# Kernel tuning notes

Hardware: AMD Instinct MI355X
Metric: run time of the kernel (lower is better)

The kernel has to match this reference:

```python
import jax, jax.numpy as jnp
import numpy as np

ANCHOR_NUM = 8
CLASS_NUM = 2
IN_DIM = 1024

def setup_inputs() -> dict:
    key = jax.random.key(0)
    k1, k2, k3, k4 = jax.random.split(key, 4)
    batch_input = jax.random.normal(k1, (64, 512, IN_DIM), dtype=jnp.float32)
    # labels in {-1, 0, 1}: -1 = padding, 0 = negative anchor, 1 = positive anchor
    anchor_labels = jax.random.randint(k2, (64, 512, ANCHOR_NUM), 0, 3, dtype=jnp.int64 if jax.config.read('jax_enable_x64') else jnp.int32) - 1
    lim = 1.0 / np.sqrt(IN_DIM)
    W = jax.random.uniform(k3, (IN_DIM, ANCHOR_NUM * CLASS_NUM), dtype=jnp.float32, minval=-lim, maxval=lim)
    b = jax.random.uniform(k4, (ANCHOR_NUM * CLASS_NUM,), dtype=jnp.float32, minval=-lim, maxval=lim)
    return {"batch_input": batch_input, "W": W, "b": b, "anchor_labels": anchor_labels}

def reference(batch_input, W, b, anchor_labels):
    B, S, _ = batch_input.shape
    # logits: (B, S, anchor_num, class_num)
    logits = (jnp.einsum('bsd,dk->bsk', batch_input, W) + b).reshape(B, S, ANCHOR_NUM, CLASS_NUM)
    predict_label = jnp.argmax(logits, axis=3)  # (B, S, A)
    valid = (anchor_labels != -1)
    labels = jnp.maximum(anchor_labels, 0)  # safe class index for padded entries
    logp = jax.nn.log_softmax(logits, axis=-1)
    nll = -jnp.take_along_axis(logp, labels[..., None].astype(jnp.int32), axis=-1)[..., 0]
    # CrossEntropyLoss (mean) over all non-padding anchors == eval-path gather + CE
    vf = valid.astype(logits.dtype)
    loss = jnp.sum(nll * vf) / jnp.maximum(jnp.sum(vf), 1.0)
    # candidate mask stands in for candidate_idx (positive predictions, non-padding)
    candidate_mask = (predict_label == 1) & valid
    return loss, predict_label, candidate_mask
```

## Files before the change

### kernel.cpp

```cpp
#include <hip/hip_runtime.h>
#include <math.h>


#define ROWS 64
#define NWAVE 4
#define DWAVE 256
#define CHUNK 32
#define XPAD 33

__global__ __launch_bounds__(256, 3)
void rpn_main(const float* __restrict__ x, const float* __restrict__ W,
              const float* __restrict__ b, const int* __restrict__ lab,
              float* __restrict__ out, float* __restrict__ ws)
{
    __shared__ float xs[NWAVE][ROWS * XPAD];
    __shared__ float red[ROWS][NWAVE * 16 + 4];

    const int tid  = threadIdx.x;
    const int wave = tid >> 6;
    const int lane = tid & 63;
    const int row0 = blockIdx.x * ROWS;

    const int uwave = __builtin_amdgcn_readfirstlane(wave);
    const float* __restrict__ Wp = W + (size_t)uwave * DWAVE * 16;

    const float* __restrict__ gbase = x + (size_t)row0 * 1024 + (size_t)wave * DWAVE;

    float acc[16];
#pragma unroll
    for (int c = 0; c < 16; ++c) acc[c] = 0.f;

    for (int ch = 0; ch < DWAVE / CHUNK; ++ch) {
        const float* gsrc = gbase + ch * CHUNK;
#pragma unroll
        for (int j = 0; j < 8; ++j) {
            int fl = j * 64 + lane;
            int r  = fl >> 3;
            int c4 = fl & 7;
            float4 v = *(const float4*)(gsrc + (size_t)r * 1024 + c4 * 4);
            float* dst = &xs[wave][r * XPAD + c4 * 4];
            dst[0] = v.x; dst[1] = v.y; dst[2] = v.z; dst[3] = v.w;
        }
        __syncthreads();

        const float* __restrict__ Wc = Wp + ch * CHUNK * 16;
        const float* xrow = &xs[wave][lane * XPAD];
#pragma unroll 4
        for (int dd = 0; dd < CHUNK; ++dd) {
            float xv = xrow[dd];
#pragma unroll
            for (int c = 0; c < 16; ++c)
                acc[c] = fmaf(xv, Wc[dd * 16 + c], acc[c]);
        }
        __syncthreads();
    }

#pragma unroll
    for (int c = 0; c < 16; c += 4) {
        float4 v = make_float4(acc[c], acc[c + 1], acc[c + 2], acc[c + 3]);
        *(float4*)&red[lane][wave * 16 + c] = v;
    }
    __syncthreads();

    if (tid < 64) {
        const int row = row0 + tid;
        float L[16];
#pragma unroll
        for (int c = 0; c < 16; ++c)
            L[c] = red[tid][c] + red[tid][16 + c] + red[tid][32 + c] + red[tid][48 + c]
                 + b[c];

        const int*  labp  = lab + (size_t)row * 8;
        float*      predp = out + 1 + (size_t)row * 8;
        float*      maskp = out + 1 + 262144 + (size_t)row * 8;

        float lsum = 0.f, lcnt = 0.f;
#pragma unroll
        for (int a = 0; a < 8; ++a) {
            float l0 = L[2 * a], l1 = L[2 * a + 1];
            int   lb = labp[a];
            int   pred  = (l1 > l0) ? 1 : 0;
            int   valid = (lb != -1);
            float m   = fmaxf(l0, l1);
            float lse = m + logf(expf(l0 - m) + expf(l1 - m));
            float nll = lse - ((lb == 1) ? l1 : l0);
            if (valid) { lsum += nll; lcnt += 1.f; }
            predp[a] = (float)pred;
            maskp[a] = (pred && valid) ? 1.f : 0.f;
        }

#pragma unroll
        for (int off = 32; off > 0; off >>= 1) {
            lsum += __shfl_down(lsum, off);
            lcnt += __shfl_down(lcnt, off);
        }
        if (tid == 0) {
            atomicAdd(&ws[0], lsum);
            atomicAdd(&ws[1], lcnt);
        }
    }
}

__global__ void rpn_final(const float* __restrict__ ws, float* __restrict__ out)
{
    out[0] = ws[0] / fmaxf(ws[1], 1.f);
}

extern "C" void kernel_launch(void* const* d_in, const int* in_sizes, int n_in,
                              void* d_out, int out_size, void* d_ws, size_t ws_size,
                              hipStream_t stream)
{
    const float* x   = (const float*)d_in[0];
    const float* W   = (const float*)d_in[1];
    const float* b   = (const float*)d_in[2];
    const int*   lab = (const int*)d_in[3];
    float* out = (float*)d_out;
    float* ws  = (float*)d_ws;

    hipMemsetAsync(ws, 0, 2 * sizeof(float), stream);
    rpn_main<<<dim3(512), dim3(256), 0, stream>>>(x, W, b, lab, out, ws);
    rpn_final<<<dim3(1), dim3(1), 0, stream>>>(ws, out);
}
```

Before: 234.4 us.

## Halve rows per block, split output columns across half-waves, stage W in LDS

Each block now handles 32 rows instead of 64, and the grid doubles to 1024 blocks. Within a wave, the two 32-lane halves each compute 8 of the 16 logit columns for the same row. W chunks are staged into shared memory and read with vectorized float4 loads, and the x tile is stored and read as float4 with a stride of 36. The goal is more blocks and occupancy to pull more memory bandwidth from this memory-bound 128MB read, and fewer scalar LDS and W loads; the cost is W being reloaded into LDS by every block.

```diff
diff --git a/kernel.cpp b/kernel.cpp
--- a/kernel.cpp
+++ b/kernel.cpp
@@ -2,77 +2,95 @@
 #include <math.h>
 
 
-#define ROWS 64
-#define NWAVE 4
-#define DWAVE 256
-#define CHUNK 32
-#define XPAD 33
+#define ROWS   32
+#define NW     4
+#define KSLICE 256
+#define CHUNK  32
+#define XSTR   36
 
-__global__ __launch_bounds__(256, 3)
+__global__ __launch_bounds__(256, 4)
 void rpn_main(const float* __restrict__ x, const float* __restrict__ W,
               const float* __restrict__ b, const int* __restrict__ lab,
               float* __restrict__ out, float* __restrict__ ws)
 {
-    __shared__ float xs[NWAVE][ROWS * XPAD];
-    __shared__ float red[ROWS][NWAVE * 16 + 4];
+    __shared__ float xs[NW * ROWS * XSTR];
+    __shared__ float wch[NW * CHUNK * 16];
+    float* red = xs;
 
     const int tid  = threadIdx.x;
     const int wave = tid >> 6;
     const int lane = tid & 63;
+    const int r    = lane & 31;
+    const int h    = lane >> 5;
     const int row0 = blockIdx.x * ROWS;
 
-    const int uwave = __builtin_amdgcn_readfirstlane(wave);
-    const float* __restrict__ Wp = W + (size_t)uwave * DWAVE * 16;
+    float* xslab = xs + wave * (ROWS * XSTR);
+    const float* gx = x + (size_t)row0 * 1024 + wave * KSLICE;
 
-    const float* __restrict__ gbase = x + (size_t)row0 * 1024 + (size_t)wave * DWAVE;
+    float acc[8];
+#pragma unroll
+    for (int c = 0; c < 8; ++c) acc[c] = 0.f;
 
-    float acc[16];
+    for (int ch = 0; ch < KSLICE / CHUNK; ++ch) {
+        const float* gsrc = gx + ch * CHUNK;
 #pragma unroll
-    for (int c = 0; c < 16; ++c) acc[c] = 0.f;
-
-    for (int ch = 0; ch < DWAVE / CHUNK; ++ch) {
-        const float* gsrc = gbase + ch * CHUNK;
+        for (int j = 0; j < 4; ++j) {
+            int fl = j * 64 + lane;
+            int rr = fl >> 3;
+            int c4 = fl & 7;
+            float4 v = *(const float4*)(gsrc + (size_t)rr * 1024 + c4 * 4);
+            *(float4*)(xslab + rr * XSTR + c4 * 4) = v;
+        }
 #pragma unroll
-        for (int j = 0; j < 8; ++j) {
-            int fl = j * 64 + lane;
-            int r  = fl >> 3;
-            int c4 = fl & 7;
-            float4 v = *(const float4*)(gsrc + (size_t)r * 1024 + c4 * 4);
-            float* dst = &xs[wave][r * XPAD + c4 * 4];
-            dst[0] = v.x; dst[1] = v.y; dst[2] = v.z; dst[3] = v.w;
+        for (int j = 0; j < 2; ++j) {
+            int e = (tid + 256 * j) * 4;
+            float4 wv = *(const float4*)(W + e + (e >> 9) * 3584 + ch * 512);
+            *(float4*)(wch + e) = wv;
         }
         __syncthreads();
 
-        const float* __restrict__ Wc = Wp + ch * CHUNK * 16;
-        const float* xrow = &xs[wave][lane * XPAD];
-#pragma unroll 4
-        for (int dd = 0; dd < CHUNK; ++dd) {
-            float xv = xrow[dd];
+        const float* xrow = xslab + r * XSTR;
+        const float* wp   = wch + wave * (CHUNK * 16) + h * 8;
 #pragma unroll
-            for (int c = 0; c < 16; ++c)
-                acc[c] = fmaf(xv, Wc[dd * 16 + c], acc[c]);
+        for (int t4 = 0; t4 < 8; ++t4) {
+            float4 xq = *(const float4*)(xrow + t4 * 4);
+#pragma unroll
+            for (int i = 0; i < 4; ++i) {
+                int dd = t4 * 4 + i;
+                float xv = (&xq.x)[i];
+                float4 w0 = *(const float4*)(wp + dd * 16);
+                float4 w1 = *(const float4*)(wp + dd * 16 + 4);
+                acc[0] = fmaf(xv, w0.x, acc[0]);
+                acc[1] = fmaf(xv, w0.y, acc[1]);
+                acc[2] = fmaf(xv, w0.z, acc[2]);
+                acc[3] = fmaf(xv, w0.w, acc[3]);
+                acc[4] = fmaf(xv, w1.x, acc[4]);
+                acc[5] = fmaf(xv, w1.y, acc[5]);
+                acc[6] = fmaf(xv, w1.z, acc[6]);
+                acc[7] = fmaf(xv, w1.w, acc[7]);
+            }
         }
         __syncthreads();
     }
 
-#pragma unroll
-    for (int c = 0; c < 16; c += 4) {
-        float4 v = make_float4(acc[c], acc[c + 1], acc[c + 2], acc[c + 3]);
-        *(float4*)&red[lane][wave * 16 + c] = v;
+    {
+        float* rp = red + r * 68 + wave * 16 + h * 8;
+        *(float4*)(rp)     = make_float4(acc[0], acc[1], acc[2], acc[3]);
+        *(float4*)(rp + 4) = make_float4(acc[4], acc[5], acc[6], acc[7]);
     }
     __syncthreads();
 
-    if (tid < 64) {
+    if (tid < ROWS) {
         const int row = row0 + tid;
         float L[16];
 #pragma unroll
         for (int c = 0; c < 16; ++c)
-            L[c] = red[tid][c] + red[tid][16 + c] + red[tid][32 + c] + red[tid][48 + c]
-                 + b[c];
+            L[c] = red[tid * 68 + c] + red[tid * 68 + 16 + c]
+                 + red[tid * 68 + 32 + c] + red[tid * 68 + 48 + c] + b[c];
 
-        const int*  labp  = lab + (size_t)row * 8;
-        float*      predp = out + 1 + (size_t)row * 8;
-        float*      maskp = out + 1 + 262144 + (size_t)row * 8;
+        const int* labp  = lab + (size_t)row * 8;
+        float*     predp = out + 1 + (size_t)row * 8;
+        float*     maskp = out + 1 + 262144 + (size_t)row * 8;
 
         float lsum = 0.f, lcnt = 0.f;
 #pragma unroll
@@ -90,9 +108,9 @@
         }
 
 #pragma unroll
-        for (int off = 32; off > 0; off >>= 1) {
-            lsum += __shfl_down(lsum, off);
-            lcnt += __shfl_down(lcnt, off);
+        for (int off = 16; off > 0; off >>= 1) {
+            lsum += __shfl_down(lsum, off, 32);
+            lcnt += __shfl_down(lcnt, off, 32);
         }
         if (tid == 0) {
             atomicAdd(&ws[0], lsum);
@@ -118,6 +136,6 @@
     float* ws  = (float*)d_ws;
 
     hipMemsetAsync(ws, 0, 2 * sizeof(float), stream);
-    rpn_main<<<dim3(512), dim3(256), 0, stream>>>(x, W, b, lab, out, ws);
+    rpn_main<<<dim3(1024), dim3(256), 0, stream>>>(x, W, b, lab, out, ws);
     rpn_final<<<dim3(1), dim3(1), 0, stream>>>(ws, out);
 }
```

After: 217.5 us. -7.2%, faster.

## Retile GEMV into 32-row blocks with register prefetch and LDS-staged W

Applied to the files above, without the earlier changes.

Restructures the matmul so each block handles 32 rows across the full K dimension in 128-wide chunks. Each thread computes an 8x8 register tile using float4 LDS reads, W is staged in LDS, and the next x chunk is prefetched into registers while the current one is computed. The grid doubles to 1024 blocks, and cross-thread K partials are combined with LDS atomics. The epilogue uses all 256 threads, one per anchor, with a block-level loss reduction before the global atomic. The aim is more memory-level parallelism and fewer LDS reads per FMA on a bandwidth-bound 128MB read, at the cost of many LDS float atomics.

```diff
diff --git a/kernel.cpp b/kernel.cpp
--- a/kernel.cpp
+++ b/kernel.cpp
@@ -2,102 +2,129 @@
 #include <math.h>
 
 
-#define ROWS 64
-#define NWAVE 4
-#define DWAVE 256
-#define CHUNK 32
-#define XPAD 33
+#define ROWS 32
+#define CK   128
+#define NCH  8
 
-__global__ __launch_bounds__(256, 3)
+__global__ __launch_bounds__(256, 4)
 void rpn_main(const float* __restrict__ x, const float* __restrict__ W,
               const float* __restrict__ b, const int* __restrict__ lab,
               float* __restrict__ out, float* __restrict__ ws)
 {
-    __shared__ float xs[NWAVE][ROWS * XPAD];
-    __shared__ float red[ROWS][NWAVE * 16 + 4];
+    __shared__ __align__(16) float xs[ROWS * CK];
+    __shared__ __align__(16) float wlds[CK * 16];
+    __shared__ float red[ROWS * 16];
+    __shared__ float lossred[2];
 
-    const int tid  = threadIdx.x;
-    const int wave = tid >> 6;
-    const int lane = tid & 63;
+    const int tid = threadIdx.x;
+    const int g   = tid >> 3;
+    const int rg  = (tid & 7) >> 1;
+    const int cg  = tid & 1;
     const int row0 = blockIdx.x * ROWS;
 
-    const int uwave = __builtin_amdgcn_readfirstlane(wave);
-    const float* __restrict__ Wp = W + (size_t)uwave * DWAVE * 16;
+    red[tid]       = b[tid & 15];
+    red[tid + 256] = b[tid & 15];
+    if (tid < 2) lossred[tid] = 0.f;
 
-    const float* __restrict__ gbase = x + (size_t)row0 * 1024 + (size_t)wave * DWAVE;
+    const float* gx = x + (size_t)row0 * 1024;
 
-    float acc[16];
+    float acc[8][8];
 #pragma unroll
-    for (int c = 0; c < 16; ++c) acc[c] = 0.f;
+    for (int i = 0; i < 8; ++i)
+#pragma unroll
+        for (int c = 0; c < 8; ++c) acc[i][c] = 0.f;
 
-    for (int ch = 0; ch < DWAVE / CHUNK; ++ch) {
-        const float* gsrc = gbase + ch * CHUNK;
+    float4 xv[4];
 #pragma unroll
-        for (int j = 0; j < 8; ++j) {
-            int fl = j * 64 + lane;
-            int r  = fl >> 3;
-            int c4 = fl & 7;
-            float4 v = *(const float4*)(gsrc + (size_t)r * 1024 + c4 * 4);
-            float* dst = &xs[wave][r * XPAD + c4 * 4];
-            dst[0] = v.x; dst[1] = v.y; dst[2] = v.z; dst[3] = v.w;
+    for (int j = 0; j < 4; ++j) {
+        int fl = j * 256 + tid;
+        xv[j] = *(const float4*)(gx + (size_t)(fl >> 5) * 1024 + (fl & 31) * 4);
+    }
+
+    for (int c = 0; c < NCH; ++c) {
+        __syncthreads();
+#pragma unroll
+        for (int j = 0; j < 4; ++j)
+            *(float4*)(xs + (j * 256 + tid) * 4) = xv[j];
+#pragma unroll
+        for (int j = 0; j < 2; ++j) {
+            int fl = j * 256 + tid;
+            float4 wv = *(const float4*)(W + c * (CK * 16) + fl * 4);
+            *(float4*)(wlds + fl * 4) = wv;
         }
         __syncthreads();
-
-        const float* __restrict__ Wc = Wp + ch * CHUNK * 16;
-        const float* xrow = &xs[wave][lane * XPAD];
-#pragma unroll 4
-        for (int dd = 0; dd < CHUNK; ++dd) {
-            float xv = xrow[dd];
+        if (c + 1 < NCH) {
 #pragma unroll
-            for (int c = 0; c < 16; ++c)
-                acc[c] = fmaf(xv, Wc[dd * 16 + c], acc[c]);
+            for (int j = 0; j < 4; ++j) {
+                int fl = j * 256 + tid;
+                xv[j] = *(const float4*)(gx + (size_t)(fl >> 5) * 1024
+                                            + (c + 1) * CK + (fl & 31) * 4);
+            }
         }
-        __syncthreads();
+        const float* xp = xs + rg * CK + g * 4;
+        const float* wp = wlds + g * 64 + cg * 8;
+        float4 wa[4], wb[4];
+#pragma unroll
+        for (int dk = 0; dk < 4; ++dk) {
+            wa[dk] = *(const float4*)(wp + dk * 16);
+            wb[dk] = *(const float4*)(wp + dk * 16 + 4);
+        }
+#pragma unroll
+        for (int i = 0; i < 8; ++i) {
+            float4 xq = *(const float4*)(xp + i * (4 * CK));
+            float xk[4] = {xq.x, xq.y, xq.z, xq.w};
+#pragma unroll
+            for (int dk = 0; dk < 4; ++dk) {
+                acc[i][0] = fmaf(xk[dk], wa[dk].x, acc[i][0]);
+                acc[i][1] = fmaf(xk[dk], wa[dk].y, acc[i][1]);
+                acc[i][2] = fmaf(xk[dk], wa[dk].z, acc[i][2]);
+                acc[i][3] = fmaf(xk[dk], wa[dk].w, acc[i][3]);
+                acc[i][4] = fmaf(xk[dk], wb[dk].x, acc[i][4]);
+                acc[i][5] = fmaf(xk[dk], wb[dk].y, acc[i][5]);
+                acc[i][6] = fmaf(xk[dk], wb[dk].z, acc[i][6]);
+                acc[i][7] = fmaf(xk[dk], wb[dk].w, acc[i][7]);
+            }
+        }
     }
 
 #pragma unroll
-    for (int c = 0; c < 16; c += 4) {
-        float4 v = make_float4(acc[c], acc[c + 1], acc[c + 2], acc[c + 3]);
-        *(float4*)&red[lane][wave * 16 + c] = v;
+    for (int i = 0; i < 8; ++i) {
+        int rbase = (rg + 4 * i) * 16 + cg * 8;
+#pragma unroll
+        for (int cc = 0; cc < 8; ++cc)
+            atomicAdd(&red[rbase + cc], acc[i][cc]);
     }
     __syncthreads();
 
-    if (tid < 64) {
-        const int row = row0 + tid;
-        float L[16];
-#pragma unroll
-        for (int c = 0; c < 16; ++c)
-            L[c] = red[tid][c] + red[tid][16 + c] + red[tid][32 + c] + red[tid][48 + c]
-                 + b[c];
-
-        const int*  labp  = lab + (size_t)row * 8;
-        float*      predp = out + 1 + (size_t)row * 8;
-        float*      maskp = out + 1 + 262144 + (size_t)row * 8;
-
-        float lsum = 0.f, lcnt = 0.f;
-#pragma unroll
-        for (int a = 0; a < 8; ++a) {
-            float l0 = L[2 * a], l1 = L[2 * a + 1];
-            int   lb = labp[a];
-            int   pred  = (l1 > l0) ? 1 : 0;
-            int   valid = (lb != -1);
-            float m   = fmaxf(l0, l1);
-            float lse = m + logf(expf(l0 - m) + expf(l1 - m));
-            float nll = lse - ((lb == 1) ? l1 : l0);
-            if (valid) { lsum += nll; lcnt += 1.f; }
-            predp[a] = (float)pred;
-            maskp[a] = (pred && valid) ? 1.f : 0.f;
-        }
-
+    {
+        const int row = tid >> 3;
+        const int a   = tid & 7;
+        float2 l01 = *(const float2*)&red[row * 16 + 2 * a];
+        int lb = lab[(size_t)row0 * 8 + tid];
+        float l0 = l01.x, l1 = l01.y;
+        int pred  = (l1 > l0) ? 1 : 0;
+        int valid = (lb != -1);
+        float m   = fmaxf(l0, l1);
+        float lse = m + logf(expf(l0 - m) + expf(l1 - m));
+        float nll = lse - ((lb == 1) ? l1 : l0);
+        float ls = valid ? nll : 0.f;
+        float lc = valid ? 1.f : 0.f;
+        out[1 + (size_t)row0 * 8 + tid] = (float)pred;
+        out[1 + 262144 + (size_t)row0 * 8 + tid] = (pred && valid) ? 1.f : 0.f;
 #pragma unroll
         for (int off = 32; off > 0; off >>= 1) {
-            lsum += __shfl_down(lsum, off);
-            lcnt += __shfl_down(lcnt, off);
+            ls += __shfl_down(ls, off);
+            lc += __shfl_down(lc, off);
         }
-        if (tid == 0) {
-            atomicAdd(&ws[0], lsum);
-            atomicAdd(&ws[1], lcnt);
+        if ((tid & 63) == 0) {
+            atomicAdd(&lossred[0], ls);
+            atomicAdd(&lossred[1], lc);
         }
+    }
+    __syncthreads();
+    if (tid == 0) {
+        atomicAdd(&ws[0], lossred[0]);
+        atomicAdd(&ws[1], lossred[1]);
     }
 }
 
@@ -118,6 +145,6 @@
     float* ws  = (float*)d_ws;
 
     hipMemsetAsync(ws, 0, 2 * sizeof(float), stream);
-    rpn_main<<<dim3(512), dim3(256), 0, stream>>>(x, W, b, lab, out, ws);
+    rpn_main<<<dim3(1024), dim3(256), 0, stream>>>(x, W, b, lab, out, ws);
     rpn_final<<<dim3(1), dim3(1), 0, stream>>>(ws, out);
 }
```

After: 342.2 us. +46.0%, slower.
